# Optimization experiments

Measured on AMD Instinct MI355X. Metric: run time of the kernel, lower is better.

Reference implementation:

```python
import jax, jax.numpy as jnp
import numpy as np

NUM_EMBEDDINGS = 1024
EMBEDDING_DIM = 256
SPLIT = 8
SPLIT_DIM = EMBEDDING_DIM // SPLIT  # 32
COMMITMENT_COST = 0.25
DECAY = 0.99
EPSILON = 1e-05


def setup_inputs() -> dict:
    key = jax.random.key(0)
    k1, k2, k3 = jax.random.split(key, 3)
    inputs = jax.random.normal(k1, (16384, EMBEDDING_DIM), dtype=jnp.float32)
    embedding = jax.random.normal(k2, (NUM_EMBEDDINGS, SPLIT_DIM), dtype=jnp.float32)
    ema_cluster_size = jnp.zeros((NUM_EMBEDDINGS,), dtype=jnp.float32)
    ema_w = jax.random.normal(k3, (NUM_EMBEDDINGS, SPLIT_DIM), dtype=jnp.float32)
    return {"inputs": inputs, "embedding": embedding,
            "ema_cluster_size": ema_cluster_size, "ema_w": ema_w}


def reference(inputs, embedding, ema_cluster_size, ema_w):
    B = inputs.shape[0]
    flat = inputs.reshape(-1, SPLIT_DIM)  # [B*split, d]
    rows = flat.shape[0]

    # squared euclidean distances to codebook: [rows, K]
    distances = (jnp.sum(flat ** 2, axis=1, keepdims=True)
                 + jnp.sum(embedding ** 2, axis=1)
                 - 2.0 * flat @ embedding.T)
    idx = jnp.argmin(distances, axis=1)  # [rows]

    # one-hot @ embedding == gather (same math, efficient form)
    quantized_flat = embedding[idx]  # [rows, d]

    # EMA statistics (training-mode update); quantization uses the OLD weights,
    # exactly as in the torch forward.
    counts = jax.ops.segment_sum(jnp.ones((rows,), jnp.float32), idx,
                                 num_segments=NUM_EMBEDDINGS)
    dw = jax.ops.segment_sum(flat, idx, num_segments=NUM_EMBEDDINGS)  # enc.T @ flat
    new_cs = ema_cluster_size * DECAY + (1.0 - DECAY) * counts
    n = jnp.sum(new_cs)
    new_cs = (new_cs + EPSILON) / (n + NUM_EMBEDDINGS * EPSILON) * n
    new_ema_w = ema_w * DECAY + (1.0 - DECAY) * dw
    new_embedding = new_ema_w / new_cs[:, None]

    # losses (EMA variant: only commitment term)
    e_latent_loss = jnp.mean((jax.lax.stop_gradient(quantized_flat) - flat) ** 2)
    loss = COMMITMENT_COST * e_latent_loss

    # straight-through estimator
    quantized_flat = flat + jax.lax.stop_gradient(quantized_flat - flat)
    quantized = quantized_flat.reshape(B, -1)  # [B, EMBEDDING_DIM]

    avg_probs = counts / rows  # mean of one-hot encodings over rows
    perplexity = jnp.exp(-jnp.sum(avg_probs * jnp.log(avg_probs + 1e-10)))

    encoding_indices = idx.reshape(B, SPLIT)
    return (loss, quantized, perplexity, encoding_indices,
            new_embedding, new_cs, new_ema_w)
```

## Files before the change

### kernel.cpp

```cpp
#include <hip/hip_runtime.h>

#define NUM_CODES 1024
#define DIM 32
#define ROWS 131072
#define DECAYF 0.99f
#define EPSF 1e-5f
#define CCOST 0.25f
#define SLAB 33792
#define RGROUPS 4
#define IBLK (SLAB / 256)
#define TILES_PER_CHUNK 16
#define DBIAS 256.0f

typedef __attribute__((ext_vector_type(8))) short short8v;
typedef __attribute__((ext_vector_type(4))) float f32x4;

__device__ __forceinline__ unsigned short bf16_rne(float f) {
    unsigned u = __float_as_uint(f);
    unsigned r = u + 0x7FFFu + ((u >> 16) & 1u);
    return (unsigned short)(r >> 16);
}

__global__ __launch_bounds__(256) void k_prep(const float* __restrict__ emb,
                                              unsigned short* __restrict__ bhi,
                                              unsigned short* __restrict__ blo,
                                              float* __restrict__ nbias,
                                              float* __restrict__ sumf2) {
    int s = blockIdx.x * 256 + threadIdx.x;
    if (s == 0) sumf2[0] = 0.0f;
    if (s < NUM_CODES) {
        const float4* e4 = (const float4*)(emb + s * DIM);
        float sum = 0.0f;
#pragma unroll
        for (int j = 0; j < 8; ++j) {
            float4 e = e4[j];
            sum += e.x * e.x + e.y * e.y + e.z * e.z + e.w * e.w;
        }
        nbias[s] = -0.5f * sum - DBIAS;
    }
    int l = s & 63, t = s >> 6;
    int code = t * 16 + (l & 15);
    int koff = (l >> 4) * 8;
    const float* src = emb + code * DIM + koff;
    float4 f0 = *(const float4*)(src);
    float4 f1 = *(const float4*)(src + 4);
    float fv[8] = {f0.x, f0.y, f0.z, f0.w, f1.x, f1.y, f1.z, f1.w};
    short8v h, lo;
#pragma unroll
    for (int j = 0; j < 8; ++j) {
        unsigned short hb = bf16_rne(fv[j]);
        float hf = __uint_as_float((unsigned)hb << 16);
        h[j]  = (short)hb;
        lo[j] = (short)bf16_rne(fv[j] - hf);
    }
    *(short8v*)(bhi + (size_t)s * 8) = h;
    *(short8v*)(blo + (size_t)s * 8) = lo;
}

__global__ __launch_bounds__(256) void k_argmin(const float* __restrict__ flat,
                                                const unsigned short* __restrict__ bhi_g,
                                                const unsigned short* __restrict__ blo_g,
                                                const float* __restrict__ nbias,
                                                const float* __restrict__ emb,
                                                int* __restrict__ idx_out,
                                                float* __restrict__ idxf_out,
                                                float* __restrict__ qout) {
    __shared__ unsigned win[4][32];
    __shared__ int kwin[32];
    const int lane = threadIdx.x & 63;
    const int wid  = threadIdx.x >> 6;
    const int rowbase = blockIdx.x * 32;
    const int lr = lane & 15;
    const int lg = lane >> 4;

    short8v ahi[2], alo[2];
#pragma unroll
    for (int rf = 0; rf < 2; ++rf) {
        const float* src = flat + (size_t)(rowbase + rf * 16 + lr) * DIM + lg * 8;
        float4 f0 = *(const float4*)src;
        float4 f1 = *(const float4*)(src + 4);
        float fv[8] = {f0.x, f0.y, f0.z, f0.w, f1.x, f1.y, f1.z, f1.w};
        short8v h, lo;
#pragma unroll
        for (int j = 0; j < 8; ++j) {
            unsigned short hb = bf16_rne(fv[j]);
            float hf = __uint_as_float((unsigned)hb << 16);
            h[j]  = (short)hb;
            lo[j] = (short)bf16_rne(fv[j] - hf);
        }
        ahi[rf] = h; alo[rf] = lo;
    }

    unsigned best[2][4];
#pragma unroll
    for (int rf = 0; rf < 2; ++rf)
#pragma unroll
        for (int rg = 0; rg < 4; ++rg) best[rf][rg] = 0xFFFFFFFFu;

    const int t0 = wid * TILES_PER_CHUNK;
#pragma unroll 2
    for (int tt = 0; tt < TILES_PER_CHUNK; ++tt) {
        const int t = t0 + tt;
        short8v bh = *(const short8v*)(bhi_g + ((size_t)t * 64 + lane) * 8);
        short8v bl = *(const short8v*)(blo_g + ((size_t)t * 64 + lane) * 8);
        float nn = nbias[t * 16 + lr];
        unsigned code = (unsigned)(t * 16 + lr);
#pragma unroll
        for (int rf = 0; rf < 2; ++rf) {
            f32x4 acc = {nn, nn, nn, nn};
            acc = __builtin_amdgcn_mfma_f32_16x16x32_bf16(ahi[rf], bh, acc, 0, 0, 0);
            acc = __builtin_amdgcn_mfma_f32_16x16x32_bf16(ahi[rf], bl, acc, 0, 0, 0);
            acc = __builtin_amdgcn_mfma_f32_16x16x32_bf16(alo[rf], bh, acc, 0, 0, 0);
#pragma unroll
            for (int rg = 0; rg < 4; ++rg) {
                unsigned pb = (__float_as_uint(acc[rg]) & 0xFFFFFC00u) | code;
                best[rf][rg] = min(best[rf][rg], pb);
            }
        }
    }

#pragma unroll
    for (int rf = 0; rf < 2; ++rf) {
#pragma unroll
        for (int rg = 0; rg < 4; ++rg) {
            unsigned b = best[rf][rg];
#pragma unroll
            for (int m = 1; m < 16; m <<= 1)
                b = min(b, (unsigned)__shfl_xor((int)b, m));
            if (lr == rg) win[wid][rf * 16 + lg * 4 + rg] = b;
        }
    }
    __syncthreads();

    if (threadIdx.x < 32) {
        unsigned pm = min(min(win[0][threadIdx.x], win[1][threadIdx.x]),
                          min(win[2][threadIdx.x], win[3][threadIdx.x]));
        int k = (int)(pm & 1023u);
        kwin[threadIdx.x] = k;
        idx_out[rowbase + threadIdx.x]  = k;
        idxf_out[rowbase + threadIdx.x] = (float)k;
    }
    __syncthreads();

    {
        int row = threadIdx.x >> 3, seg = threadIdx.x & 7;
        int k = kwin[row];
        float4 e = *(const float4*)(emb + (size_t)k * DIM + seg * 4);
        *(float4*)(qout + (size_t)(rowbase + row) * DIM + seg * 4) = e;
    }
}

__global__ __launch_bounds__(256) void k_scatter(const float* __restrict__ flat,
                                                 const int* __restrict__ idx,
                                                 float* __restrict__ slabs,
                                                 float* __restrict__ sumf2,
                                                 int rows_per_block) {
    __shared__ float acc[SLAB];
    __shared__ float red[256];
    const int tid = threadIdx.x;
    for (int i = tid; i < SLAB; i += 256) acc[i] = 0.0f;
    __syncthreads();

    const int row0 = blockIdx.x * rows_per_block;
    float sf = 0.0f;
    for (int rr = 0; rr < rows_per_block; rr += 256) {
        int r = row0 + rr + tid;
        int k = idx[r];
        const float4* f4 = (const float4*)(flat + (size_t)r * DIM);
        int kb = k * DIM;
#pragma unroll
        for (int j4 = 0; j4 < 8; ++j4) {
            float4 f = f4[j4];
            sf += f.x * f.x + f.y * f.y + f.z * f.z + f.w * f.w;
            int j = 4 * j4;
            atomicAdd(&acc[kb + ((j + 0 + k) & 31)], f.x);
            atomicAdd(&acc[kb + ((j + 1 + k) & 31)], f.y);
            atomicAdd(&acc[kb + ((j + 2 + k) & 31)], f.z);
            atomicAdd(&acc[kb + ((j + 3 + k) & 31)], f.w);
        }
        atomicAdd(&acc[32768 + k], 1.0f);
    }
    __syncthreads();

    float* slab = slabs + (size_t)blockIdx.x * SLAB;
    for (int i = tid; i < 32768; i += 256) {
        int k = i >> 5, j = i & 31;
        slab[i] = acc[(i & ~31) | ((j + k) & 31)];
    }
    for (int i = tid; i < NUM_CODES; i += 256) slab[32768 + i] = acc[32768 + i];

    red[tid] = sf;
    __syncthreads();
    for (int s = 128; s > 0; s >>= 1) {
        if (tid < s) red[tid] += red[tid + s];
        __syncthreads();
    }
    if (tid == 0) atomicAdd(sumf2, red[0]);
}

__global__ __launch_bounds__(256) void k_reduce1(const float* __restrict__ slabs,
                                                 float* __restrict__ partial,
                                                 int pcount) {
    int g  = blockIdx.x / IBLK;
    int ib = blockIdx.x % IBLK;
    int i = ib * 256 + threadIdx.x;
    const float* base = slabs + (size_t)g * pcount * SLAB + i;
    float s = 0.0f;
#pragma unroll 4
    for (int p = 0; p < pcount; ++p) s += base[(size_t)p * SLAB];
    partial[(size_t)g * SLAB + i] = s;
}

__global__ __launch_bounds__(1024) void k_final(const float* __restrict__ ema_cs,
                                                const float* __restrict__ ema_w,
                                                const float* __restrict__ emb,
                                                const float* __restrict__ partial,
                                                const float* __restrict__ sumf2,
                                                float* __restrict__ out_loss,
                                                float* __restrict__ out_perp,
                                                float* __restrict__ out_emb,
                                                float* __restrict__ out_cs,
                                                float* __restrict__ out_ema_w) {
    int tid = threadIdx.x;
    __shared__ float s_cs[NUM_CODES];
    __shared__ float s_cnt[NUM_CODES];
    __shared__ float red[1024];
    __shared__ double redd[1024];

    float c = 0.0f;
#pragma unroll
    for (int g = 0; g < RGROUPS; ++g) c += partial[(size_t)g * SLAB + 32768 + tid];
    s_cnt[tid] = c;
    float pre = ema_cs[tid] * DECAYF + (1.0f - DECAYF) * c;

    red[tid] = pre;
    __syncthreads();
    for (int s = 512; s > 0; s >>= 1) {
        if (tid < s) red[tid] += red[tid + s];
        __syncthreads();
    }
    float n = red[0];
    __syncthreads();

    float ncs = (pre + EPSF) / (n + (float)NUM_CODES * EPSF) * n;
    s_cs[tid] = ncs;
    out_cs[tid] = ncs;

    float p = c / (float)ROWS;
    red[tid] = p * logf(p + 1e-10f);
    __syncthreads();
    for (int s = 512; s > 0; s >>= 1) {
        if (tid < s) red[tid] += red[tid + s];
        __syncthreads();
    }
    float nplogp = red[0];
    __syncthreads();

    double lterm = 0.0;
    for (int i = tid; i < NUM_CODES * DIM; i += 1024) {
        int k = i >> 5;
        float dwv = 0.0f;
#pragma unroll
        for (int g = 0; g < RGROUPS; ++g) dwv += partial[(size_t)g * SLAB + i];
        float e = emb[i];
        lterm += (double)e * ((double)e * (double)s_cnt[k] - 2.0 * (double)dwv);
        float w = ema_w[i] * DECAYF + (1.0f - DECAYF) * dwv;
        out_ema_w[i] = w;
        out_emb[i] = w / s_cs[k];
    }
    redd[tid] = lterm;
    __syncthreads();
    for (int s = 512; s > 0; s >>= 1) {
        if (tid < s) redd[tid] += redd[tid + s];
        __syncthreads();
    }
    if (tid == 0) {
        double lsum = (double)sumf2[0] + redd[0];
        out_loss[0] = (float)(CCOST * lsum / (double)((size_t)ROWS * DIM));
        out_perp[0] = expf(-nplogp);
    }
}

extern "C" void kernel_launch(void* const* d_in, const int* in_sizes, int n_in,
                              void* d_out, int out_size, void* d_ws, size_t ws_size,
                              hipStream_t stream) {
    const float* inputs    = (const float*)d_in[0];
    const float* embedding = (const float*)d_in[1];
    const float* ema_cs    = (const float*)d_in[2];
    const float* ema_w     = (const float*)d_in[3];

    float* out        = (float*)d_out;
    float* out_loss   = out;
    float* out_q      = out + 1;
    float* out_perp   = out + 4194305;
    float* out_idxf   = out + 4194306;
    float* out_emb    = out + 4325378;
    float* out_cs     = out + 4358146;
    float* out_ema_w  = out + 4359170;

    char* ws = (char*)d_ws;
    float* nbias      = (float*)(ws);
    float* sumf2      = (float*)(ws + 4096);
    int*   idx        = (int*)(ws + 8192);
    unsigned short* bhi_g = (unsigned short*)(ws + 532480);
    unsigned short* blo_g = (unsigned short*)(ws + 598016);
    float* partial    = (float*)(ws + 663552);
    float* slabs      = (float*)(ws + 1204224);

    size_t slab_off = 1204224;
    size_t avail = (ws_size > slab_off) ? (ws_size - slab_off) : 0;
    int P = 16;
    if (avail >= (size_t)256 * SLAB * 4) P = 256;
    else if (avail >= (size_t)128 * SLAB * 4) P = 128;
    else if (avail >= (size_t)64 * SLAB * 4) P = 64;
    else if (avail >= (size_t)32 * SLAB * 4) P = 32;
    int rows_per_block = ROWS / P;

    k_prep   <<<16, 256, 0, stream>>>(embedding, bhi_g, blo_g, nbias, sumf2);
    k_argmin <<<ROWS / 32, 256, 0, stream>>>(inputs, bhi_g, blo_g, nbias, embedding,
                                             idx, out_idxf, out_q);
    k_scatter<<<P, 256, 0, stream>>>(inputs, idx, slabs, sumf2, rows_per_block);
    k_reduce1<<<RGROUPS * IBLK, 256, 0, stream>>>(slabs, partial, P / RGROUPS);
    k_final  <<<1, 1024, 0, stream>>>(ema_cs, ema_w, embedding, partial, sumf2,
                                      out_loss, out_perp, out_emb, out_cs, out_ema_w);
}
```

Before: 109.9 us.

## Double argmin rows per block, prefetch codebook tiles, cap scatter slabs

The argmin kernel now handles 64 rows per block with four A fragments per wave, so each loaded codebook tile is reused across twice as many MFMA row groups. The next tile's bf16 hi/lo and bias are register-prefetched during the current tile's MFMAs, and the tile loop is fully unrolled. The scatter stage is limited to at most 64 slabs, and the two-level reduction becomes a single reduce kernel that writes dw and counts directly for the final kernel. This costs more registers in argmin and halves its grid, and the scatter stage gets less parallelism.

```diff
diff --git a/kernel.cpp b/kernel.cpp
--- a/kernel.cpp
+++ b/kernel.cpp
@@ -7,7 +7,6 @@
 #define EPSF 1e-5f
 #define CCOST 0.25f
 #define SLAB 33792
-#define RGROUPS 4
 #define IBLK (SLAB / 256)
 #define TILES_PER_CHUNK 16
 #define DBIAS 256.0f
@@ -65,17 +64,17 @@
                                                 int* __restrict__ idx_out,
                                                 float* __restrict__ idxf_out,
                                                 float* __restrict__ qout) {
-    __shared__ unsigned win[4][32];
-    __shared__ int kwin[32];
+    __shared__ unsigned win[4][64];
+    __shared__ int kwin[64];
     const int lane = threadIdx.x & 63;
     const int wid  = threadIdx.x >> 6;
-    const int rowbase = blockIdx.x * 32;
+    const int rowbase = blockIdx.x * 64;
     const int lr = lane & 15;
     const int lg = lane >> 4;
 
-    short8v ahi[2], alo[2];
-#pragma unroll
-    for (int rf = 0; rf < 2; ++rf) {
+    short8v ahi[4], alo[4];
+#pragma unroll
+    for (int rf = 0; rf < 4; ++rf) {
         const float* src = flat + (size_t)(rowbase + rf * 16 + lr) * DIM + lg * 8;
         float4 f0 = *(const float4*)src;
         float4 f1 = *(const float4*)(src + 4);
@@ -91,26 +90,35 @@
         ahi[rf] = h; alo[rf] = lo;
     }
 
-    unsigned best[2][4];
-#pragma unroll
-    for (int rf = 0; rf < 2; ++rf)
+    unsigned best[4][4];
+#pragma unroll
+    for (int rf = 0; rf < 4; ++rf)
 #pragma unroll
         for (int rg = 0; rg < 4; ++rg) best[rf][rg] = 0xFFFFFFFFu;
 
     const int t0 = wid * TILES_PER_CHUNK;
-#pragma unroll 2
+    const short8v* bhp = (const short8v*)(bhi_g + ((size_t)t0 * 64 + lane) * 8);
+    const short8v* blp = (const short8v*)(blo_g + ((size_t)t0 * 64 + lane) * 8);
+    short8v bh = bhp[0];
+    short8v bl = blp[0];
+    float   nn = nbias[t0 * 16 + lr];
+
+#pragma unroll
     for (int tt = 0; tt < TILES_PER_CHUNK; ++tt) {
-        const int t = t0 + tt;
-        short8v bh = *(const short8v*)(bhi_g + ((size_t)t * 64 + lane) * 8);
-        short8v bl = *(const short8v*)(blo_g + ((size_t)t * 64 + lane) * 8);
-        float nn = nbias[t * 16 + lr];
-        unsigned code = (unsigned)(t * 16 + lr);
-#pragma unroll
-        for (int rf = 0; rf < 2; ++rf) {
-            f32x4 acc = {nn, nn, nn, nn};
-            acc = __builtin_amdgcn_mfma_f32_16x16x32_bf16(ahi[rf], bh, acc, 0, 0, 0);
-            acc = __builtin_amdgcn_mfma_f32_16x16x32_bf16(ahi[rf], bl, acc, 0, 0, 0);
-            acc = __builtin_amdgcn_mfma_f32_16x16x32_bf16(alo[rf], bh, acc, 0, 0, 0);
+        short8v bhc = bh, blc = bl;
+        float nnc = nn;
+        unsigned code = (unsigned)((t0 + tt) * 16 + lr);
+        if (tt + 1 < TILES_PER_CHUNK) {
+            bh = bhp[(tt + 1) * 64];
+            bl = blp[(tt + 1) * 64];
+            nn = nbias[(t0 + tt + 1) * 16 + lr];
+        }
+#pragma unroll
+        for (int rf = 0; rf < 4; ++rf) {
+            f32x4 acc = {nnc, nnc, nnc, nnc};
+            acc = __builtin_amdgcn_mfma_f32_16x16x32_bf16(ahi[rf], bhc, acc, 0, 0, 0);
+            acc = __builtin_amdgcn_mfma_f32_16x16x32_bf16(ahi[rf], blc, acc, 0, 0, 0);
+            acc = __builtin_amdgcn_mfma_f32_16x16x32_bf16(alo[rf], bhc, acc, 0, 0, 0);
 #pragma unroll
             for (int rg = 0; rg < 4; ++rg) {
                 unsigned pb = (__float_as_uint(acc[rg]) & 0xFFFFFC00u) | code;
@@ -120,7 +128,7 @@
     }
 
 #pragma unroll
-    for (int rf = 0; rf < 2; ++rf) {
+    for (int rf = 0; rf < 4; ++rf) {
 #pragma unroll
         for (int rg = 0; rg < 4; ++rg) {
             unsigned b = best[rf][rg];
@@ -132,7 +140,7 @@
     }
     __syncthreads();
 
-    if (threadIdx.x < 32) {
+    if (threadIdx.x < 64) {
         unsigned pm = min(min(win[0][threadIdx.x], win[1][threadIdx.x]),
                           min(win[2][threadIdx.x], win[3][threadIdx.x]));
         int k = (int)(pm & 1023u);
@@ -142,8 +150,9 @@
     }
     __syncthreads();
 
-    {
-        int row = threadIdx.x >> 3, seg = threadIdx.x & 7;
+#pragma unroll
+    for (int h = 0; h < 2; ++h) {
+        int row = h * 32 + (threadIdx.x >> 3), seg = threadIdx.x & 7;
         int k = kwin[row];
         float4 e = *(const float4*)(emb + (size_t)k * DIM + seg * 4);
         *(float4*)(qout + (size_t)(rowbase + row) * DIM + seg * 4) = e;
@@ -198,23 +207,22 @@
     if (tid == 0) atomicAdd(sumf2, red[0]);
 }
 
-__global__ __launch_bounds__(256) void k_reduce1(const float* __restrict__ slabs,
-                                                 float* __restrict__ partial,
-                                                 int pcount) {
-    int g  = blockIdx.x / IBLK;
-    int ib = blockIdx.x % IBLK;
-    int i = ib * 256 + threadIdx.x;
-    const float* base = slabs + (size_t)g * pcount * SLAB + i;
+__global__ __launch_bounds__(256) void k_reduce(const float* __restrict__ slabs,
+                                                float* __restrict__ dw_sum,
+                                                float* __restrict__ counts_sum,
+                                                int P) {
+    int i = blockIdx.x * 256 + threadIdx.x;
     float s = 0.0f;
-#pragma unroll 4
-    for (int p = 0; p < pcount; ++p) s += base[(size_t)p * SLAB];
-    partial[(size_t)g * SLAB + i] = s;
+    for (int p = 0; p < P; ++p) s += slabs[(size_t)p * SLAB + i];
+    if (i < 32768) dw_sum[i] = s;
+    else           counts_sum[i - 32768] = s;
 }
 
 __global__ __launch_bounds__(1024) void k_final(const float* __restrict__ ema_cs,
                                                 const float* __restrict__ ema_w,
                                                 const float* __restrict__ emb,
-                                                const float* __restrict__ partial,
+                                                const float* __restrict__ counts,
+                                                const float* __restrict__ dw,
                                                 const float* __restrict__ sumf2,
                                                 float* __restrict__ out_loss,
                                                 float* __restrict__ out_perp,
@@ -227,9 +235,7 @@
     __shared__ float red[1024];
     __shared__ double redd[1024];
 
-    float c = 0.0f;
-#pragma unroll
-    for (int g = 0; g < RGROUPS; ++g) c += partial[(size_t)g * SLAB + 32768 + tid];
+    float c = counts[tid];
     s_cnt[tid] = c;
     float pre = ema_cs[tid] * DECAYF + (1.0f - DECAYF) * c;
 
@@ -259,9 +265,7 @@
     double lterm = 0.0;
     for (int i = tid; i < NUM_CODES * DIM; i += 1024) {
         int k = i >> 5;
-        float dwv = 0.0f;
-#pragma unroll
-        for (int g = 0; g < RGROUPS; ++g) dwv += partial[(size_t)g * SLAB + i];
+        float dwv = dw[i];
         float e = emb[i];
         lterm += (double)e * ((double)e * (double)s_cnt[k] - 2.0 * (double)dwv);
         float w = ema_w[i] * DECAYF + (1.0f - DECAYF) * dwv;
@@ -304,23 +308,23 @@
     int*   idx        = (int*)(ws + 8192);
     unsigned short* bhi_g = (unsigned short*)(ws + 532480);
     unsigned short* blo_g = (unsigned short*)(ws + 598016);
-    float* partial    = (float*)(ws + 663552);
-    float* slabs      = (float*)(ws + 1204224);
-
-    size_t slab_off = 1204224;
+    float* dw_sum     = (float*)(ws + 663552);
+    float* counts_sum = (float*)(ws + 794624);
+    float* slabs      = (float*)(ws + 798720);
+
+    size_t slab_off = 798720;
     size_t avail = (ws_size > slab_off) ? (ws_size - slab_off) : 0;
     int P = 16;
-    if (avail >= (size_t)256 * SLAB * 4) P = 256;
-    else if (avail >= (size_t)128 * SLAB * 4) P = 128;
-    else if (avail >= (size_t)64 * SLAB * 4) P = 64;
+    if (avail >= (size_t)64 * SLAB * 4) P = 64;
     else if (avail >= (size_t)32 * SLAB * 4) P = 32;
     int rows_per_block = ROWS / P;
 
     k_prep   <<<16, 256, 0, stream>>>(embedding, bhi_g, blo_g, nbias, sumf2);
-    k_argmin <<<ROWS / 32, 256, 0, stream>>>(inputs, bhi_g, blo_g, nbias, embedding,
+    k_argmin <<<ROWS / 64, 256, 0, stream>>>(inputs, bhi_g, blo_g, nbias, embedding,
                                              idx, out_idxf, out_q);
     k_scatter<<<P, 256, 0, stream>>>(inputs, idx, slabs, sumf2, rows_per_block);
-    k_reduce1<<<RGROUPS * IBLK, 256, 0, stream>>>(slabs, partial, P / RGROUPS);
-    k_final  <<<1, 1024, 0, stream>>>(ema_cs, ema_w, embedding, partial, sumf2,
-                                      out_loss, out_perp, out_emb, out_cs, out_ema_w);
-}
+    k_reduce <<<IBLK, 256, 0, stream>>>(slabs, dw_sum, counts_sum, P);
+    k_final  <<<1, 1024, 0, stream>>>(ema_cs, ema_w, embedding, counts_sum, dw_sum,
+                                      sumf2, out_loss, out_perp, out_emb, out_cs,
+                                      out_ema_w);
+}
```

After: 206.2 us. +87.6%, slower.
